# Kernel tuning notes

Measured on AMD Instinct MI355X. Metric: run time of the kernel, lower is better.

Reference implementation:

```python
import jax, jax.numpy as jnp
import numpy as np

B, L, S, H, E = 4, 1024, 1024, 8, 64


def setup_inputs() -> dict:
    key = jax.random.key(0)
    ks = jax.random.split(key, 8)
    return {
        "query": jax.random.normal(ks[0], (B, L, H, E), dtype=jnp.float32),
        "key": jax.random.normal(ks[1], (B, S, H, E), dtype=jnp.float32),
        "value": jax.random.normal(ks[2], (B, S, H, E), dtype=jnp.float32),
        "phi": jax.random.normal(ks[3], (H, L, S), dtype=jnp.float32),
        "log_gain": jnp.asarray(np.log(10.0), dtype=jnp.float32),
        "log_tau": jnp.asarray(np.log(2.0), dtype=jnp.float32),
        "log_tau_comm": jnp.asarray(np.log(0.2), dtype=jnp.float32),
        "hard_mask": jax.random.uniform(ks[4], (L, S), dtype=jnp.float32),
        "u": jax.random.uniform(ks[5], (H, L, S), dtype=jnp.float32),
        "mask_miss_k": jnp.ones((B, S), dtype=jnp.float32),
        "mask_miss_q": jnp.ones((B, L), dtype=jnp.float32),
        "pos": jnp.zeros((B, L), dtype=jnp.float32),
        "causal_mask": 0,
    }


def reference(query, key, value, phi, log_gain, log_tau, log_tau_comm,
              hard_mask, u, mask_miss_k, mask_miss_q, pos, causal_mask):
    # mask_miss_k/q, pos, causal_mask are unused by LieAttention.forward (torch parity)
    E_dim = query.shape[-1]
    scale = 1.0 / float(np.sqrt(E_dim))
    # raw scores (B, H, L, S)
    scores = jnp.einsum('blhe,bshe->bhls', query, key)
    # antisymmetric communication term
    comm = scores - jnp.swapaxes(scores, -1, -2)
    gain = jnp.clip(jnp.exp(log_gain), 1e-3, 1000.0)      # max_gain = 1000
    tau_comm = jnp.clip(jnp.exp(log_tau_comm), 1e-3, 10.0)
    comm_amp = jnp.tanh((gain / tau_comm) * comm)
    att = scale * jax.nn.gelu(comm_amp, approximate=False)  # torch F.gelu = exact erf
    # Gumbel-sigmoid relaxed DAG mask, broadcast over batch: M (1, H, L, S)
    tau = jnp.clip(jnp.exp(log_tau), 0.1, 5.0)             # tau_min/tau_max
    m_relaxed = jax.nn.sigmoid((jnp.log(u + 1e-8) - jnp.log(1.0 - u + 1e-8) + phi) / tau)
    att = att * m_relaxed[None]
    # hard mask (L, S) -> (1, 1, L, S)
    att = att * hard_mask[None, None]
    # attention entropy per query position: (B, H, L)
    eps = 1e-8
    entropy = jnp.nan_to_num(-jnp.sum(att * jnp.log(jnp.maximum(att, eps)), axis=-1))
    A = jnp.nan_to_num(att)  # dropout=0.0 -> identity
    V = jnp.einsum('bhls,bshd->blhd', A, value)
    return V, A, entropy
```

## Files before the change

kernel.cpp:

```cpp
#include <hip/hip_runtime.h>
#include <math.h>

#define Bn 4
#define Ln 1024
#define Sn 1024
#define Hn 8
#define En 64

typedef __attribute__((ext_vector_type(4))) float f32x4;
typedef __attribute__((ext_vector_type(8))) short s16x8;
typedef __attribute__((ext_vector_type(4))) short s16x4;

__device__ __forceinline__ short f2bf(float x) {
    unsigned u = __float_as_uint(x);
    unsigned r = (u + 0x7FFFu + ((u >> 16) & 1u)) >> 16;
    return (short)r;
}
__device__ __forceinline__ float bf2f(short s) {
    return __uint_as_float(((unsigned)(unsigned short)s) << 16);
}
__device__ __forceinline__ float frcp(float x) { return __builtin_amdgcn_rcpf(x); }

__global__ __launch_bounds__(256, 2) void fused_lie(
    const float* __restrict__ Q, const float* __restrict__ K,
    const float* __restrict__ V, const float* __restrict__ phi,
    const float* __restrict__ u, const float* __restrict__ hard,
    const float* __restrict__ p_lg, const float* __restrict__ p_lt,
    const float* __restrict__ p_ltc,
    float* __restrict__ Aout, float* __restrict__ Vout,
    float* __restrict__ entOut) {
    __shared__ __align__(16) short kbh[64 * 72];
    __shared__ __align__(16) short kbl[64 * 72];
    __shared__ __align__(16) short qbh[64 * 72];
    __shared__ __align__(16) short qbl[64 * 72];
    __shared__ __align__(16) short vbt[64 * 72];
    __shared__ __align__(16) short plds[4][16 * 72];

    const int lt = blockIdx.x, h = blockIdx.y, b = blockIdx.z;
    const int tid = threadIdx.x;
    const int w = tid >> 6;
    const int lane = tid & 63;
    const int q = lane >> 4;
    const int n = lane & 15;
    const int l0 = lt * 64;

    const float gain = fminf(fmaxf(expf(p_lg[0]), 1e-3f), 1000.0f);
    const float tauc = fminf(fmaxf(expf(p_ltc[0]), 1e-3f), 10.0f);
    const float c1 = gain / tauc;
    const float tau = fminf(fmaxf(expf(p_lt[0]), 0.1f), 5.0f);
    const float itau = 1.0f / tau;

    s16x8 QAh[2], QAl[2], KAh[2], KAl[2];
    {
        const int la = l0 + w * 16 + n;
        const float* qrow = Q + (((size_t)b * Ln + la) * Hn + h) * En;
        const float* krow = K + (((size_t)b * Sn + la) * Hn + h) * En;
#pragma unroll
        for (int kh = 0; kh < 2; ++kh) {
            const int e0 = q * 8 + kh * 32;
            float qe[8], ke[8];
            *(f32x4*)(qe) = *(const f32x4*)(qrow + e0);
            *(f32x4*)(qe + 4) = *(const f32x4*)(qrow + e0 + 4);
            *(f32x4*)(ke) = *(const f32x4*)(krow + e0);
            *(f32x4*)(ke + 4) = *(const f32x4*)(krow + e0 + 4);
            s16x8 qh8, ql8, kh8, kl8;
#pragma unroll
            for (int j = 0; j < 8; ++j) {
                short hq = f2bf(qe[j]);
                qh8[j] = hq; ql8[j] = f2bf(qe[j] - bf2f(hq));
                float nk = -ke[j];
                short hk = f2bf(nk);
                kh8[j] = hk; kl8[j] = f2bf(nk - bf2f(hk));
            }
            QAh[kh] = qh8; QAl[kh] = ql8; KAh[kh] = kh8; KAl[kh] = kl8;
        }
    }

    f32x4 accV[4];
#pragma unroll
    for (int i = 0; i < 4; ++i) accV[i] = (f32x4){0.f, 0.f, 0.f, 0.f};
    float entp[4] = {0.f, 0.f, 0.f, 0.f};

    for (int st = 0; st < 16; ++st) {
        const int s0 = st * 64;
        if (st) __syncthreads();

#pragma unroll
        for (int i = 0; i < 4; ++i) {
            int idx = tid + 256 * i;
            int row = idx >> 4;
            int c4 = (idx & 15) << 2;
            f32x4 kv = *(const f32x4*)(K + (((size_t)b * Sn + s0 + row) * Hn + h) * En + c4);
            f32x4 qv = *(const f32x4*)(Q + (((size_t)b * Ln + s0 + row) * Hn + h) * En + c4);
            s16x4 kh4, kl4, qh4, ql4;
#pragma unroll
            for (int j = 0; j < 4; ++j) {
                short t = f2bf(kv[j]); kh4[j] = t; kl4[j] = f2bf(kv[j] - bf2f(t));
                short t2 = f2bf(qv[j]); qh4[j] = t2; ql4[j] = f2bf(qv[j] - bf2f(t2));
            }
            int o = row * 72 + c4;
            *(s16x4*)&kbh[o] = kh4; *(s16x4*)&kbl[o] = kl4;
            *(s16x4*)&qbh[o] = qh4; *(s16x4*)&qbl[o] = ql4;
        }
#pragma unroll
        for (int i = 0; i < 4; ++i) {
            int sg = (tid >> 6) + 4 * i;
            int d = tid & 63;
            s16x4 vv;
#pragma unroll
            for (int jj = 0; jj < 4; ++jj) {
                float x = V[(((size_t)b * Sn + s0 + sg * 4 + jj) * Hn + h) * En + d];
                vv[jj] = f2bf(x);
            }
            *(s16x4*)&vbt[d * 72 + sg * 4] = vv;
        }
        __syncthreads();

        f32x4 acc[4];
#pragma unroll
        for (int i = 0; i < 4; ++i) acc[i] = (f32x4){0.f, 0.f, 0.f, 0.f};
#pragma unroll
        for (int kh = 0; kh < 2; ++kh) {
#pragma unroll
            for (int sub = 0; sub < 4; ++sub) {
                const int off = (sub * 16 + n) * 72 + q * 8 + kh * 32;
                s16x8 KBh = *(const s16x8*)&kbh[off];
                s16x8 KBl = *(const s16x8*)&kbl[off];
                s16x8 QBh = *(const s16x8*)&qbh[off];
                s16x8 QBl = *(const s16x8*)&qbl[off];
                f32x4 a = acc[sub];
                a = __builtin_amdgcn_mfma_f32_16x16x32_bf16(QAh[kh], KBh, a, 0, 0, 0);
                a = __builtin_amdgcn_mfma_f32_16x16x32_bf16(QAh[kh], KBl, a, 0, 0, 0);
                a = __builtin_amdgcn_mfma_f32_16x16x32_bf16(QAl[kh], KBh, a, 0, 0, 0);
                a = __builtin_amdgcn_mfma_f32_16x16x32_bf16(KAh[kh], QBh, a, 0, 0, 0);
                a = __builtin_amdgcn_mfma_f32_16x16x32_bf16(KAh[kh], QBl, a, 0, 0, 0);
                a = __builtin_amdgcn_mfma_f32_16x16x32_bf16(KAl[kh], QBh, a, 0, 0, 0);
                acc[sub] = a;
            }
        }

        const int lbase = l0 + w * 16 + q * 4;
#pragma unroll
        for (int sub = 0; sub < 4; ++sub) {
            const int s = s0 + sub * 16 + n;
#pragma unroll
            for (int r = 0; r < 4; ++r) {
                const int l = lbase + r;
                const size_t pidx = ((size_t)h * Ln + l) * (size_t)Sn + s;
                float ph = phi[pidx];
                float uu = u[pidx];
                float hm = hard[(size_t)l * Sn + s];
                float cm = acc[sub][r];
                float e2 = __expf(2.0f * c1 * cm);
                float x = 1.0f - 2.0f * frcp(e2 + 1.0f);
                float g = 0.5f * x * (1.0f + erff(x * 0.70710678118654752f));
                float z = (__logf((uu + 1e-8f) * frcp(1.0f - uu + 1e-8f)) + ph) * itau;
                float m = frcp(1.0f + __expf(-z));
                float att = 0.125f * g * m * hm;
                Aout[(((size_t)b * Hn + h) * Ln + l) * (size_t)Sn + s] = att;
                entp[r] += att * __logf(fmaxf(att, 1e-8f));
                plds[w][(q * 4 + r) * 72 + sub * 16 + n] = f2bf(att);
            }
        }

        {
            const short* pw = &plds[w][0];
#pragma unroll
            for (int kh = 0; kh < 2; ++kh) {
                s16x8 Pf = *(const s16x8*)&pw[n * 72 + q * 8 + kh * 32];
#pragma unroll
                for (int sub = 0; sub < 4; ++sub) {
                    s16x8 Vf = *(const s16x8*)&vbt[(sub * 16 + n) * 72 + q * 8 + kh * 32];
                    accV[sub] = __builtin_amdgcn_mfma_f32_16x16x32_bf16(Pf, Vf, accV[sub], 0, 0, 0);
                }
            }
        }
    }

#pragma unroll
    for (int sub = 0; sub < 4; ++sub) {
#pragma unroll
        for (int r = 0; r < 4; ++r) {
            const int l = l0 + w * 16 + q * 4 + r;
            Vout[(((size_t)b * Ln + l) * Hn + h) * En + sub * 16 + n] = accV[sub][r];
        }
    }
#pragma unroll
    for (int r = 0; r < 4; ++r) {
        float v = entp[r];
        v += __shfl_xor(v, 1);
        v += __shfl_xor(v, 2);
        v += __shfl_xor(v, 4);
        v += __shfl_xor(v, 8);
        if (n == 0) {
            float e = -v;
            if (!(e == e)) e = 0.f;
            entOut[((size_t)b * Hn + h) * Ln + l0 + w * 16 + q * 4 + r] = e;
        }
    }
}

extern "C" void kernel_launch(void* const* d_in, const int* in_sizes, int n_in,
                              void* d_out, int out_size, void* d_ws, size_t ws_size,
                              hipStream_t stream) {
    (void)in_sizes; (void)n_in; (void)d_ws; (void)ws_size; (void)out_size;

    const float* Q    = (const float*)d_in[0];
    const float* K    = (const float*)d_in[1];
    const float* Vv   = (const float*)d_in[2];
    const float* phi  = (const float*)d_in[3];
    const float* lg   = (const float*)d_in[4];
    const float* ltau = (const float*)d_in[5];
    const float* ltc  = (const float*)d_in[6];
    const float* hard = (const float*)d_in[7];
    const float* u    = (const float*)d_in[8];

    float* out  = (float*)d_out;
    float* Vout = out;
    float* Aout = out + (size_t)Bn * Ln * Hn * En;
    float* ent  = Aout + (size_t)Bn * Hn * Ln * Sn;

    fused_lie<<<dim3(16, Hn, Bn), 256, 0, stream>>>(Q, K, Vv, phi, u, hard,
                                                    lg, ltau, ltc, Aout, Vout, ent);
}
```

Baseline: 362.9 us.

## Precompute fp16 hi/lo Q/K/V in prep kernel, split S across blocks with atomics

Adds a prep kernel that converts Q, K and V once into split fp16 hi/lo arrays with XOR-swizzled layouts, stored in workspace. The main kernel then streams tiles into LDS with global_load_lds instead of converting per tile. It also splits the S range across two blocks per L-tile, accumulating V and entropy with atomicAdd after memsets. Other changes: switching from bf16 to fp16 MFMA, replacing erf GELU with a tanh-style sigmoid approximation, and raising the occupancy hint. This trades extra launches, atomics, a changed GELU approximation and dropped NaN handling for less redundant conversion work and more parallelism.

```diff
diff --git a/kernel.cpp b/kernel.cpp
--- a/kernel.cpp
+++ b/kernel.cpp
@@ -8,71 +8,114 @@
 #define En 64
 
 typedef __attribute__((ext_vector_type(4))) float f32x4;
-typedef __attribute__((ext_vector_type(8))) short s16x8;
-typedef __attribute__((ext_vector_type(4))) short s16x4;
-
-__device__ __forceinline__ short f2bf(float x) {
-    unsigned u = __float_as_uint(x);
-    unsigned r = (u + 0x7FFFu + ((u >> 16) & 1u)) >> 16;
-    return (short)r;
-}
-__device__ __forceinline__ float bf2f(short s) {
-    return __uint_as_float(((unsigned)(unsigned short)s) << 16);
-}
+typedef __attribute__((ext_vector_type(8))) _Float16 h16x8;
+typedef __attribute__((ext_vector_type(4))) _Float16 h16x4;
+
 __device__ __forceinline__ float frcp(float x) { return __builtin_amdgcn_rcpf(x); }
 
-__global__ __launch_bounds__(256, 2) void fused_lie(
+__device__ __forceinline__ void gl_lds16(const void* g, void* l) {
+    __builtin_amdgcn_global_load_lds(
+        (const __attribute__((address_space(1))) unsigned int*)g,
+        (__attribute__((address_space(3))) unsigned int*)l, 16, 0, 0);
+}
+
+__global__ __launch_bounds__(256) void prep(
     const float* __restrict__ Q, const float* __restrict__ K,
-    const float* __restrict__ V, const float* __restrict__ phi,
-    const float* __restrict__ u, const float* __restrict__ hard,
+    const float* __restrict__ V,
+    _Float16* __restrict__ Qh, _Float16* __restrict__ Ql,
+    _Float16* __restrict__ Kh, _Float16* __restrict__ Kl,
+    _Float16* __restrict__ Vt) {
+    __shared__ float vlds[64][69];
+    const int st = blockIdx.x;
+    const int bh = blockIdx.y;
+    const int b = bh >> 3, h = bh & 7;
+    const int tid = threadIdx.x;
+    const int s0 = st * 64;
+
+#pragma unroll
+    for (int i = 0; i < 4; ++i) {
+        int idx = tid + 256 * i;
+        int r = idx >> 4;
+        int c4 = (idx & 15) << 2;
+        size_t gin = (((size_t)b * Ln + s0 + r) * Hn + h) * En + c4;
+        f32x4 qv = *(const f32x4*)(Q + gin);
+        f32x4 kv = *(const f32x4*)(K + gin);
+        f32x4 vv = *(const f32x4*)(V + gin);
+        vlds[r][c4 + 0] = vv.x; vlds[r][c4 + 1] = vv.y;
+        vlds[r][c4 + 2] = vv.z; vlds[r][c4 + 3] = vv.w;
+        h16x4 qh4, ql4, kh4, kl4;
+#pragma unroll
+        for (int j = 0; j < 4; ++j) {
+            float x = qv[j];
+            _Float16 hx = (_Float16)x;
+            qh4[j] = hx; ql4[j] = (_Float16)(x - (float)hx);
+            float y = kv[j];
+            _Float16 hy = (_Float16)y;
+            kh4[j] = hy; kl4[j] = (_Float16)(y - (float)hy);
+        }
+        size_t ob = ((size_t)bh * 1024 + s0 + r) * 64 + ((((c4 >> 3) ^ (r & 7)) << 3) + (c4 & 7));
+        *(h16x4*)(Qh + ob) = qh4; *(h16x4*)(Ql + ob) = ql4;
+        *(h16x4*)(Kh + ob) = kh4; *(h16x4*)(Kl + ob) = kl4;
+    }
+    __syncthreads();
+#pragma unroll
+    for (int i = 0; i < 4; ++i) {
+        int idx = tid + 256 * i;
+        int d = idx >> 4;
+        int sg = (idx & 15) << 2;
+        h16x4 v4;
+#pragma unroll
+        for (int j = 0; j < 4; ++j) v4[j] = (_Float16)vlds[sg + j][d];
+        size_t ob = (((size_t)bh * 16 + st) * 64 + d) * 64 + ((((sg >> 3) ^ (d & 7)) << 3) + (sg & 7));
+        *(h16x4*)(Vt + ob) = v4;
+    }
+}
+
+__global__ __launch_bounds__(256, 3) void fused_lie(
+    const _Float16* __restrict__ Qh, const _Float16* __restrict__ Ql,
+    const _Float16* __restrict__ Kh, const _Float16* __restrict__ Kl,
+    const _Float16* __restrict__ Vt,
+    const float* __restrict__ phi, const float* __restrict__ u,
+    const float* __restrict__ hard,
     const float* __restrict__ p_lg, const float* __restrict__ p_lt,
     const float* __restrict__ p_ltc,
     float* __restrict__ Aout, float* __restrict__ Vout,
     float* __restrict__ entOut) {
-    __shared__ __align__(16) short kbh[64 * 72];
-    __shared__ __align__(16) short kbl[64 * 72];
-    __shared__ __align__(16) short qbh[64 * 72];
-    __shared__ __align__(16) short qbl[64 * 72];
-    __shared__ __align__(16) short vbt[64 * 72];
-    __shared__ __align__(16) short plds[4][16 * 72];
-
-    const int lt = blockIdx.x, h = blockIdx.y, b = blockIdx.z;
+    __shared__ __align__(16) _Float16 kbh[4096];
+    __shared__ __align__(16) _Float16 kbl[4096];
+    __shared__ __align__(16) _Float16 qbh[4096];
+    __shared__ __align__(16) _Float16 qbl[4096];
+    __shared__ __align__(16) _Float16 vbt[4096];
+    __shared__ __align__(16) _Float16 plds[4][16 * 72];
+
+    const int bx = blockIdx.x;
+    const int lt = bx >> 1, sh = bx & 1;
+    const int h = blockIdx.y, b = blockIdx.z;
+    const int bh = b * Hn + h;
     const int tid = threadIdx.x;
     const int w = tid >> 6;
     const int lane = tid & 63;
     const int q = lane >> 4;
     const int n = lane & 15;
+    const int swz = n & 7;
     const int l0 = lt * 64;
 
     const float gain = fminf(fmaxf(expf(p_lg[0]), 1e-3f), 1000.0f);
     const float tauc = fminf(fmaxf(expf(p_ltc[0]), 1e-3f), 10.0f);
-    const float c1 = gain / tauc;
+    const float c2 = 2.0f * gain / tauc;
     const float tau = fminf(fmaxf(expf(p_lt[0]), 0.1f), 5.0f);
     const float itau = 1.0f / tau;
 
-    s16x8 QAh[2], QAl[2], KAh[2], KAl[2];
+    h16x8 QAh[2], QAl[2], KAh[2], KAl[2];
     {
-        const int la = l0 + w * 16 + n;
-        const float* qrow = Q + (((size_t)b * Ln + la) * Hn + h) * En;
-        const float* krow = K + (((size_t)b * Sn + la) * Hn + h) * En;
+        const size_t ab = ((size_t)bh * 1024 + l0 + w * 16 + n) * 64;
 #pragma unroll
         for (int kh = 0; kh < 2; ++kh) {
-            const int e0 = q * 8 + kh * 32;
-            float qe[8], ke[8];
-            *(f32x4*)(qe) = *(const f32x4*)(qrow + e0);
-            *(f32x4*)(qe + 4) = *(const f32x4*)(qrow + e0 + 4);
-            *(f32x4*)(ke) = *(const f32x4*)(krow + e0);
-            *(f32x4*)(ke + 4) = *(const f32x4*)(krow + e0 + 4);
-            s16x8 qh8, ql8, kh8, kl8;
-#pragma unroll
-            for (int j = 0; j < 8; ++j) {
-                short hq = f2bf(qe[j]);
-                qh8[j] = hq; ql8[j] = f2bf(qe[j] - bf2f(hq));
-                float nk = -ke[j];
-                short hk = f2bf(nk);
-                kh8[j] = hk; kl8[j] = f2bf(nk - bf2f(hk));
-            }
-            QAh[kh] = qh8; QAl[kh] = ql8; KAh[kh] = kh8; KAl[kh] = kl8;
+            size_t off = ab + (((q + kh * 4) ^ swz) << 3);
+            QAh[kh] = *(const h16x8*)(Qh + off);
+            QAl[kh] = *(const h16x8*)(Ql + off);
+            KAh[kh] = *(const h16x8*)(Kh + off);
+            KAl[kh] = *(const h16x8*)(Kl + off);
         }
     }
 
@@ -81,65 +124,54 @@
     for (int i = 0; i < 4; ++i) accV[i] = (f32x4){0.f, 0.f, 0.f, 0.f};
     float entp[4] = {0.f, 0.f, 0.f, 0.f};
 
-    for (int st = 0; st < 16; ++st) {
+    const int lbase = l0 + w * 16 + q * 4;
+
+    for (int stc = 0; stc < 8; ++stc) {
+        const int st = sh * 8 + stc;
         const int s0 = st * 64;
-        if (st) __syncthreads();
-
+        if (stc) __syncthreads();
+
+        {
+            const size_t sb = ((size_t)bh * 1024 + s0) * 64;
+            const size_t vb = (((size_t)bh * 16 + st) * 64) * 64;
+#pragma unroll
+            for (int i = 0; i < 2; ++i) {
+                int hoff = w * 1024 + i * 512 + lane * 8;
+                gl_lds16(Kh + sb + hoff, kbh + hoff);
+                gl_lds16(Kl + sb + hoff, kbl + hoff);
+                gl_lds16(Qh + sb + hoff, qbh + hoff);
+                gl_lds16(Ql + sb + hoff, qbl + hoff);
+                gl_lds16(Vt + vb + hoff, vbt + hoff);
+            }
+        }
+        __syncthreads();
+
+        f32x4 a1[4], a2[4];
 #pragma unroll
         for (int i = 0; i < 4; ++i) {
-            int idx = tid + 256 * i;
-            int row = idx >> 4;
-            int c4 = (idx & 15) << 2;
-            f32x4 kv = *(const f32x4*)(K + (((size_t)b * Sn + s0 + row) * Hn + h) * En + c4);
-            f32x4 qv = *(const f32x4*)(Q + (((size_t)b * Ln + s0 + row) * Hn + h) * En + c4);
-            s16x4 kh4, kl4, qh4, ql4;
-#pragma unroll
-            for (int j = 0; j < 4; ++j) {
-                short t = f2bf(kv[j]); kh4[j] = t; kl4[j] = f2bf(kv[j] - bf2f(t));
-                short t2 = f2bf(qv[j]); qh4[j] = t2; ql4[j] = f2bf(qv[j] - bf2f(t2));
-            }
-            int o = row * 72 + c4;
-            *(s16x4*)&kbh[o] = kh4; *(s16x4*)&kbl[o] = kl4;
-            *(s16x4*)&qbh[o] = qh4; *(s16x4*)&qbl[o] = ql4;
-        }
-#pragma unroll
-        for (int i = 0; i < 4; ++i) {
-            int sg = (tid >> 6) + 4 * i;
-            int d = tid & 63;
-            s16x4 vv;
-#pragma unroll
-            for (int jj = 0; jj < 4; ++jj) {
-                float x = V[(((size_t)b * Sn + s0 + sg * 4 + jj) * Hn + h) * En + d];
-                vv[jj] = f2bf(x);
-            }
-            *(s16x4*)&vbt[d * 72 + sg * 4] = vv;
-        }
-        __syncthreads();
-
-        f32x4 acc[4];
-#pragma unroll
-        for (int i = 0; i < 4; ++i) acc[i] = (f32x4){0.f, 0.f, 0.f, 0.f};
+            a1[i] = (f32x4){0.f, 0.f, 0.f, 0.f};
+            a2[i] = (f32x4){0.f, 0.f, 0.f, 0.f};
+        }
 #pragma unroll
         for (int kh = 0; kh < 2; ++kh) {
 #pragma unroll
             for (int sub = 0; sub < 4; ++sub) {
-                const int off = (sub * 16 + n) * 72 + q * 8 + kh * 32;
-                s16x8 KBh = *(const s16x8*)&kbh[off];
-                s16x8 KBl = *(const s16x8*)&kbl[off];
-                s16x8 QBh = *(const s16x8*)&qbh[off];
-                s16x8 QBl = *(const s16x8*)&qbl[off];
-                f32x4 a = acc[sub];
-                a = __builtin_amdgcn_mfma_f32_16x16x32_bf16(QAh[kh], KBh, a, 0, 0, 0);
-                a = __builtin_amdgcn_mfma_f32_16x16x32_bf16(QAh[kh], KBl, a, 0, 0, 0);
-                a = __builtin_amdgcn_mfma_f32_16x16x32_bf16(QAl[kh], KBh, a, 0, 0, 0);
-                a = __builtin_amdgcn_mfma_f32_16x16x32_bf16(KAh[kh], QBh, a, 0, 0, 0);
-                a = __builtin_amdgcn_mfma_f32_16x16x32_bf16(KAh[kh], QBl, a, 0, 0, 0);
-                a = __builtin_amdgcn_mfma_f32_16x16x32_bf16(KAl[kh], QBh, a, 0, 0, 0);
-                acc[sub] = a;
-            }
-        }
-
-        const int lbase = l0 + w * 16 + q * 4;
+                const int off = (sub * 16 + n) * 64 + (((q + kh * 4) ^ swz) << 3);
+                h16x8 KBh = *(const h16x8*)&kbh[off];
+                h16x8 KBl = *(const h16x8*)&kbl[off];
+                h16x8 QBh = *(const h16x8*)&qbh[off];
+                h16x8 QBl = *(const h16x8*)&qbl[off];
+                f32x4 x1 = a1[sub], x2 = a2[sub];
+                x1 = __builtin_amdgcn_mfma_f32_16x16x32_f16(QAh[kh], KBh, x1, 0, 0, 0);
+                x1 = __builtin_amdgcn_mfma_f32_16x16x32_f16(QAh[kh], KBl, x1, 0, 0, 0);
+                x1 = __builtin_amdgcn_mfma_f32_16x16x32_f16(QAl[kh], KBh, x1, 0, 0, 0);
+                x2 = __builtin_amdgcn_mfma_f32_16x16x32_f16(KAh[kh], QBh, x2, 0, 0, 0);
+                x2 = __builtin_amdgcn_mfma_f32_16x16x32_f16(KAh[kh], QBl, x2, 0, 0, 0);
+                x2 = __builtin_amdgcn_mfma_f32_16x16x32_f16(KAl[kh], QBh, x2, 0, 0, 0);
+                a1[sub] = x1; a2[sub] = x2;
+            }
+        }
+
 #pragma unroll
         for (int sub = 0; sub < 4; ++sub) {
             const int s = s0 + sub * 16 + n;
@@ -150,28 +182,28 @@
                 float ph = phi[pidx];
                 float uu = u[pidx];
                 float hm = hard[(size_t)l * Sn + s];
-                float cm = acc[sub][r];
-                float e2 = __expf(2.0f * c1 * cm);
-                float x = 1.0f - 2.0f * frcp(e2 + 1.0f);
-                float g = 0.5f * x * (1.0f + erff(x * 0.70710678118654752f));
+                float cm = a1[sub][r] - a2[sub][r];
+                float x = 1.0f - 2.0f * frcp(__expf(c2 * cm) + 1.0f);
+                float t = x * fmaf(0.044715f * x, x, 1.0f);
+                float g = x * frcp(1.0f + __expf(-1.59576912161f * t));
                 float z = (__logf((uu + 1e-8f) * frcp(1.0f - uu + 1e-8f)) + ph) * itau;
                 float m = frcp(1.0f + __expf(-z));
                 float att = 0.125f * g * m * hm;
                 Aout[(((size_t)b * Hn + h) * Ln + l) * (size_t)Sn + s] = att;
                 entp[r] += att * __logf(fmaxf(att, 1e-8f));
-                plds[w][(q * 4 + r) * 72 + sub * 16 + n] = f2bf(att);
+                plds[w][(q * 4 + r) * 72 + sub * 16 + n] = (_Float16)att;
             }
         }
 
         {
-            const short* pw = &plds[w][0];
+            const _Float16* pw = &plds[w][0];
 #pragma unroll
             for (int kh = 0; kh < 2; ++kh) {
-                s16x8 Pf = *(const s16x8*)&pw[n * 72 + q * 8 + kh * 32];
+                h16x8 Pf = *(const h16x8*)&pw[n * 72 + q * 8 + kh * 32];
 #pragma unroll
                 for (int sub = 0; sub < 4; ++sub) {
-                    s16x8 Vf = *(const s16x8*)&vbt[(sub * 16 + n) * 72 + q * 8 + kh * 32];
-                    accV[sub] = __builtin_amdgcn_mfma_f32_16x16x32_bf16(Pf, Vf, accV[sub], 0, 0, 0);
+                    h16x8 Vf = *(const h16x8*)&vbt[(sub * 16 + n) * 64 + (((q + kh * 4) ^ swz) << 3)];
+                    accV[sub] = __builtin_amdgcn_mfma_f32_16x16x32_f16(Pf, Vf, accV[sub], 0, 0, 0);
                 }
             }
         }
@@ -182,7 +214,7 @@
 #pragma unroll
         for (int r = 0; r < 4; ++r) {
             const int l = l0 + w * 16 + q * 4 + r;
-            Vout[(((size_t)b * Ln + l) * Hn + h) * En + sub * 16 + n] = accV[sub][r];
+            atomicAdd(Vout + (((size_t)b * Ln + l) * Hn + h) * En + sub * 16 + n, accV[sub][r]);
         }
     }
 #pragma unroll
@@ -193,9 +225,7 @@
         v += __shfl_xor(v, 4);
         v += __shfl_xor(v, 8);
         if (n == 0) {
-            float e = -v;
-            if (!(e == e)) e = 0.f;
-            entOut[((size_t)b * Hn + h) * Ln + l0 + w * 16 + q * 4 + r] = e;
+            atomicAdd(entOut + ((size_t)b * Hn + h) * Ln + lbase + r, -v);
         }
     }
 }
@@ -203,7 +233,7 @@
 extern "C" void kernel_launch(void* const* d_in, const int* in_sizes, int n_in,
                               void* d_out, int out_size, void* d_ws, size_t ws_size,
                               hipStream_t stream) {
-    (void)in_sizes; (void)n_in; (void)d_ws; (void)ws_size; (void)out_size;
+    (void)in_sizes; (void)n_in; (void)ws_size; (void)out_size;
 
     const float* Q    = (const float*)d_in[0];
     const float* K    = (const float*)d_in[1];
@@ -220,6 +250,16 @@
     float* Aout = out + (size_t)Bn * Ln * Hn * En;
     float* ent  = Aout + (size_t)Bn * Hn * Ln * Sn;
 
-    fused_lie<<<dim3(16, Hn, Bn), 256, 0, stream>>>(Q, K, Vv, phi, u, hard,
+    const size_t NE = (size_t)32 * 1024 * 64;
+    _Float16* Qh = (_Float16*)d_ws;
+    _Float16* Ql = Qh + NE;
+    _Float16* Kh = Ql + NE;
+    _Float16* Kl = Kh + NE;
+    _Float16* Vt = Kl + NE;
+
+    hipMemsetAsync(Vout, 0, (size_t)Bn * Ln * Hn * En * sizeof(float), stream);
+    hipMemsetAsync(ent, 0, (size_t)Bn * Hn * Ln * sizeof(float), stream);
+    prep<<<dim3(16, 32), 256, 0, stream>>>(Q, K, Vv, Qh, Ql, Kh, Kl, Vt);
+    fused_lie<<<dim3(32, Hn, Bn), 256, 0, stream>>>(Qh, Ql, Kh, Kl, Vt, phi, u, hard,
                                                     lg, ltau, ltc, Aout, Vout, ent);
 }
```

Result: faster. 331.1 us (-8.8%).
